# Optimization experiments

Measured on AMD Instinct MI355X. Metric: run time of the kernel, lower is better.

Reference implementation:

```python
import jax, jax.numpy as jnp
import numpy as np

N_NODES = 50000
N_EDGES = 800000
IN_DIM, HID_DIM, OUT_DIM = 64, 128, 128


def _glorot(key, shape):
    fan_in, fan_out = shape[1], shape[0]
    lim = float(np.sqrt(6.0 / (fan_in + fan_out)))
    return jax.random.uniform(key, shape, jnp.float32, -lim, lim)


def setup_inputs() -> dict:
    key = jax.random.key(0)
    ks = jax.random.split(key, 8)
    x = jax.random.normal(ks[0], (N_NODES, IN_DIM), jnp.float32)
    edge_index = jax.random.randint(ks[1], (2, N_EDGES), 0, N_NODES, jnp.int64)
    return {
        "x": x,
        "edge_index": edge_index,
        # layer 1 (SAGEConv: lin_l acts on aggregated neighbors + bias, lin_r on root)
        "W1_l": _glorot(ks[2], (HID_DIM, IN_DIM)),
        "W1_r": _glorot(ks[3], (HID_DIM, IN_DIM)),
        "b1": jnp.zeros((HID_DIM,), jnp.float32),
        # layer 2
        "W2_l": _glorot(ks[4], (OUT_DIM, HID_DIM)),
        "W2_r": _glorot(ks[5], (OUT_DIM, HID_DIM)),
        "b2": jnp.zeros((OUT_DIM,), jnp.float32),
    }


def _sage_conv(x, src, dst, W_l, W_r, b):
    # mean aggregation of neighbor features: messages flow src -> dst
    msg = x[src]                                           # [E, D]
    agg = jax.ops.segment_sum(msg, dst, num_segments=N_NODES)  # [N, D]
    deg = jax.ops.segment_sum(jnp.ones((msg.shape[0],), x.dtype), dst,
                              num_segments=N_NODES)        # [N]
    mean = agg / jnp.maximum(deg, 1.0)[:, None]            # isolated nodes -> 0
    return mean @ W_l.T + x @ W_r.T + b


def reference(x, edge_index, W1_l, W1_r, b1, W2_l, W2_r, b2):
    src, dst = edge_index[0], edge_index[1]
    h = _sage_conv(x, src, dst, W1_l, W1_r, b1)
    h = jax.nn.relu(h)
    out = _sage_conv(h, src, dst, W2_l, W2_r, b2)
    return out
```

## Files before the change

### kernel.cpp

```cpp
#include <hip/hip_runtime.h>
#include <hip/hip_bf16.h>

constexpr int N  = 50000;
constexpr int E  = 800000;
constexpr int D0 = 64;
constexpr int D1 = 128;

constexpr int SB   = 7;
constexpr int SC   = 16;
constexpr int BSTR = 128;

constexpr int NPART = 8;
constexpr int PSZ   = (N + NPART - 1) / NPART;
constexpr int BPP   = 128;

typedef __attribute__((ext_vector_type(8))) short short8;
typedef __attribute__((ext_vector_type(4))) float f32x4;

__device__ __forceinline__ unsigned short bf16bits(float f) {
    __hip_bfloat16 hb = __float2bfloat16(f);
    return *reinterpret_cast<unsigned short*>(&hb);
}

__device__ __forceinline__ void acc8(float* a, const uint4 r) {
    union { unsigned u; float f; } c;
    c.u = r.x << 16;         a[0] += c.f;
    c.u = r.x & 0xffff0000u; a[1] += c.f;
    c.u = r.y << 16;         a[2] += c.f;
    c.u = r.y & 0xffff0000u; a[3] += c.f;
    c.u = r.z << 16;         a[4] += c.f;
    c.u = r.z & 0xffff0000u; a[5] += c.f;
    c.u = r.w << 16;         a[6] += c.f;
    c.u = r.w & 0xffff0000u; a[7] += c.f;
}

__global__ __launch_bounds__(256)
void k_prep(const float* __restrict__ x, unsigned short* __restrict__ xb,
            const float* __restrict__ W1l, const float* __restrict__ W1r,
            const float* __restrict__ W2l, const float* __restrict__ W2r,
            unsigned short* __restrict__ W1cat, unsigned short* __restrict__ W2cat,
            int* __restrict__ cnt8) {
    int i = blockIdx.x * blockDim.x + threadIdx.x;
    if (i < N * 8 / 4) ((int4*)cnt8)[i] = make_int4(0, 0, 0, 0);
    if (i < 128 * 128) {
        int o = i >> 7, k = i & 127;
        float v = (k < 64) ? W1l[o * 64 + k] : W1r[o * 64 + (k - 64)];
        W1cat[i] = bf16bits(v);
    }
    if (i < 128 * 256) {
        int o = i >> 8, k = i & 255;
        float v = (k < 128) ? W2l[o * 128 + k] : W2r[o * 128 + (k - 128)];
        W2cat[i] = bf16bits(v);
    }
    if (i < N * D0 / 8) {
        const float4 v0 = *(const float4*)&x[(size_t)i * 8];
        const float4 v1 = *(const float4*)&x[(size_t)i * 8 + 4];
        float f[8] = {v0.x, v0.y, v0.z, v0.w, v1.x, v1.y, v1.z, v1.w};
        unsigned short u[8];
        #pragma unroll
        for (int j = 0; j < 8; ++j) u[j] = bf16bits(f[j]);
        *(short8*)&xb[(size_t)i * 8] = *(short8*)u;
    }
}

__global__ __launch_bounds__(256)
void k_bin(const int* __restrict__ src, const int* __restrict__ dst,
           int* __restrict__ cnt8, unsigned short* __restrict__ bin) {
    const int p     = blockIdx.x & (NPART - 1);
    const int local = blockIdx.x >> 3;
    const int lo = p * PSZ;
    const int hi = min(N, lo + PSZ);

    for (int i = local * 256 + threadIdx.x; i < E / 4; i += BPP * 256) {
        const int e0 = i * 4;
        int4 d = *(const int4*)&dst[e0];
        int4 s = *(const int4*)&src[e0];
        if (d.x >= lo && d.x < hi) {
            int sb = s.x >> 13;
            int pos = atomicAdd(&cnt8[d.x * 8 + sb], 1);
            if (pos < SC) bin[(size_t)d.x * BSTR + sb * SC + pos] = (unsigned short)s.x;
        }
        if (d.y >= lo && d.y < hi) {
            int sb = s.y >> 13;
            int pos = atomicAdd(&cnt8[d.y * 8 + sb], 1);
            if (pos < SC) bin[(size_t)d.y * BSTR + sb * SC + pos] = (unsigned short)s.y;
        }
        if (d.z >= lo && d.z < hi) {
            int sb = s.z >> 13;
            int pos = atomicAdd(&cnt8[d.z * 8 + sb], 1);
            if (pos < SC) bin[(size_t)d.z * BSTR + sb * SC + pos] = (unsigned short)s.z;
        }
        if (d.w >= lo && d.w < hi) {
            int sb = s.w >> 13;
            int pos = atomicAdd(&cnt8[d.w * 8 + sb], 1);
            if (pos < SC) bin[(size_t)d.w * BSTR + sb * SC + pos] = (unsigned short)s.w;
        }
    }
}

template<int DIN, int NT, bool RELU, bool OUT_BF16>
__global__ __launch_bounds__(256)
void k_layer(const unsigned short* __restrict__ xin,
             const int* __restrict__ cnt8,
             const unsigned short* __restrict__ bin,
             const unsigned short* __restrict__ Wcat,
             const float* __restrict__ bias,
             void* __restrict__ out,
             int n_nodes) {
    constexpr int K  = 2 * DIN;
    constexpr int KP = K + 8;
    __shared__ unsigned short A[NT * KP];

    const int tid   = threadIdx.x;
    const int nbase = blockIdx.x * NT;

    constexpr int CPR = DIN / 8;
    for (int c = tid; c < NT * CPR; c += 256) {
        int row  = c / CPR;
        int col8 = (c - row * CPR) * 8;
        int n    = nbase + row;
        short8 v = (short8)0;
        if (n < n_nodes) v = *(const short8*)&xin[(size_t)n * DIN + col8];
        *(short8*)&A[row * KP + DIN + col8] = v;
    }

    {
        constexpr int GRPSZ = DIN / 8;
        constexpr int NGRP  = 256 / GRPSZ;
        constexpr int NPG   = NT / NGRP;
        const int sub      = tid & (GRPSZ - 1);
        const int gloc     = tid / GRPSZ;
        const int lane     = tid & 63;
        const int lanebase = (lane / GRPSZ) * GRPSZ;

        float a[NPG][8];
        int   dg[NPG];
        #pragma unroll
        for (int i = 0; i < NPG; ++i) {
            dg[i] = 0;
            #pragma unroll
            for (int q = 0; q < 8; ++q) a[i][q] = 0.0f;
        }

        for (int sb = 0; sb < SB; ++sb) {
            #pragma unroll
            for (int i = 0; i < NPG; ++i) {
                const int row = gloc * NPG + i;
                const int n   = nbase + row;
                if (n < n_nodes) {
                    const int raw = cnt8[n * 8 + sb];
                    dg[i] += raw;
                    const int c = min(raw, SC);
                    const size_t base = (size_t)n * BSTR + sb * SC;
                    for (int b = 0; b < c; b += GRPSZ) {
                        int nb = (b + sub < c) ? (int)bin[base + b + sub] : 0;
                        const int cc = min(GRPSZ, c - b);
                        int j = 0;
                        for (; j + 4 <= cc; j += 4) {
                            int s0 = __shfl(nb, lanebase + j + 0);
                            int s1 = __shfl(nb, lanebase + j + 1);
                            int s2 = __shfl(nb, lanebase + j + 2);
                            int s3 = __shfl(nb, lanebase + j + 3);
                            uint4 r0 = *(const uint4*)&xin[(size_t)s0 * DIN + sub * 8];
                            uint4 r1 = *(const uint4*)&xin[(size_t)s1 * DIN + sub * 8];
                            uint4 r2 = *(const uint4*)&xin[(size_t)s2 * DIN + sub * 8];
                            uint4 r3 = *(const uint4*)&xin[(size_t)s3 * DIN + sub * 8];
                            acc8(a[i], r0); acc8(a[i], r1); acc8(a[i], r2); acc8(a[i], r3);
                        }
                        for (; j < cc; ++j) {
                            int s = __shfl(nb, lanebase + j);
                            uint4 r = *(const uint4*)&xin[(size_t)s * DIN + sub * 8];
                            acc8(a[i], r);
                        }
                    }
                }
            }
            __syncthreads();
        }

        #pragma unroll
        for (int i = 0; i < NPG; ++i) {
            const int row = gloc * NPG + i;
            const float invd = 1.0f / fmaxf((float)dg[i], 1.0f);
            unsigned short u[8];
            #pragma unroll
            for (int q = 0; q < 8; ++q) u[q] = bf16bits(a[i][q] * invd);
            *(short8*)&A[row * KP + sub * 8] = *(short8*)u;
        }
    }
    __syncthreads();

    constexpr int WR  = NT / 16;
    constexpr int NCG = 4 / WR;
    constexpr int OT  = 8 / NCG;
    const int lane = tid & 63;
    const int wv   = tid >> 6;
    const int wr   = wv % WR;
    const int wc   = wv / WR;
    const int l15  = lane & 15;
    const int kseg = lane >> 4;

    f32x4 acc[OT];
    #pragma unroll
    for (int ot = 0; ot < OT; ++ot) acc[ot] = (f32x4){0.f, 0.f, 0.f, 0.f};

    #pragma unroll
    for (int kk = 0; kk < K / 32; ++kk) {
        short8 av = *(const short8*)&A[(wr * 16 + l15) * KP + kk * 32 + kseg * 8];
        #pragma unroll
        for (int ot = 0; ot < OT; ++ot) {
            const int o16 = wc * OT + ot;
            short8 b = *(const short8*)&Wcat[(size_t)(o16 * 16 + l15) * K + kk * 32 + kseg * 8];
            acc[ot] = __builtin_amdgcn_mfma_f32_16x16x32_bf16(av, b, acc[ot], 0, 0, 0);
        }
    }

    #pragma unroll
    for (int ot = 0; ot < OT; ++ot) {
        const int o  = (wc * OT + ot) * 16 + l15;
        const float bv = bias[o];
        #pragma unroll
        for (int i = 0; i < 4; ++i) {
            int n = nbase + wr * 16 + kseg * 4 + i;
            if (n < n_nodes) {
                float v = acc[ot][i] + bv;
                if constexpr (RELU) v = fmaxf(v, 0.0f);
                if constexpr (OUT_BF16) {
                    ((unsigned short*)out)[(size_t)n * 128 + o] = bf16bits(v);
                } else {
                    ((float*)out)[(size_t)n * 128 + o] = v;
                }
            }
        }
    }
}

extern "C" void kernel_launch(void* const* d_in, const int* in_sizes, int n_in,
                              void* d_out, int out_size, void* d_ws, size_t ws_size,
                              hipStream_t stream) {
    const float* x   = (const float*)d_in[0];
    const int*   ei  = (const int*)d_in[1];
    const float* W1l = (const float*)d_in[2];
    const float* W1r = (const float*)d_in[3];
    const float* b1  = (const float*)d_in[4];
    const float* W2l = (const float*)d_in[5];
    const float* W2r = (const float*)d_in[6];
    const float* b2  = (const float*)d_in[7];
    float*       out = (float*)d_out;

    const int* src = ei;
    const int* dst = ei + E;

    char* p = (char*)d_ws;
    auto alloc = [&](size_t bytes) -> char* {
        char* r = p; p += (bytes + 15) & ~(size_t)15; return r;
    };
    int*            cnt8  = (int*)alloc((size_t)N * 8 * sizeof(int));
    unsigned short* bin   = (unsigned short*)alloc((size_t)N * BSTR * 2);
    unsigned short* xb    = (unsigned short*)alloc((size_t)N * D0 * 2);
    unsigned short* h     = (unsigned short*)alloc((size_t)N * D1 * 2);
    unsigned short* W1cat = (unsigned short*)alloc(128 * 128 * 2);
    unsigned short* W2cat = (unsigned short*)alloc(128 * 256 * 2);

    k_prep<<<(N * D0 / 8 + 255) / 256, 256, 0, stream>>>(
        x, xb, W1l, W1r, W2l, W2r, W1cat, W2cat, cnt8);

    k_bin<<<NPART * BPP, 256, 0, stream>>>(src, dst, cnt8, bin);

    k_layer<D0, 64, true, true>
        <<<(N + 63) / 64, 256, 0, stream>>>(xb, cnt8, bin, W1cat, b1, h, N);

    k_layer<D1, 32, false, false>
        <<<(N + 31) / 32, 256, 0, stream>>>(h, cnt8, bin, W2cat, b2, out, N);
}
```

Measured before the change: 187.6 us.

## Compact per-node neighbor bins and drop per-subbucket block syncs in aggregation

Adds a k_compact kernel that packs each node's seven source-bucketed neighbor slots into a contiguous list and stores the total degree plus compacted length in one int. The layer kernels then gather over one contiguous list per node, with one count read per node and no __syncthreads between source buckets. This removes the fragmented short loops and the block-wide barriers, which had also kept the gathers loosely in source-bucket order across the block. The cost is an extra launch plus a strided in-place copy pass over the bin array, and some loss of that cache locality.

```diff
diff --git a/kernel.cpp b/kernel.cpp
--- a/kernel.cpp
+++ b/kernel.cpp
@@ -98,10 +98,32 @@
     }
 }
 
+__global__ __launch_bounds__(256)
+void k_compact(const int* __restrict__ cnt8, unsigned short* __restrict__ bin,
+               int* __restrict__ cntc) {
+    int n = blockIdx.x * blockDim.x + threadIdx.x;
+    if (n >= N) return;
+    unsigned short* row = bin + (size_t)n * BSTR;
+    int raw_total = 0;
+    int cur = 0;
+    #pragma unroll
+    for (int sb = 0; sb < SB; ++sb) {
+        int raw = cnt8[n * 8 + sb];
+        raw_total += raw;
+        int c = min(raw, SC);
+        int srcoff = sb * SC;
+        if (cur != srcoff) {
+            for (int j = 0; j < c; ++j) row[cur + j] = row[srcoff + j];
+        }
+        cur += c;
+    }
+    cntc[n] = raw_total | (cur << 16);
+}
+
 template<int DIN, int NT, bool RELU, bool OUT_BF16>
 __global__ __launch_bounds__(256)
 void k_layer(const unsigned short* __restrict__ xin,
-             const int* __restrict__ cnt8,
+             const int* __restrict__ cntc,
              const unsigned short* __restrict__ bin,
              const unsigned short* __restrict__ Wcat,
              const float* __restrict__ bias,
@@ -133,58 +155,45 @@
         const int lane     = tid & 63;
         const int lanebase = (lane / GRPSZ) * GRPSZ;
 
-        float a[NPG][8];
-        int   dg[NPG];
         #pragma unroll
         for (int i = 0; i < NPG; ++i) {
-            dg[i] = 0;
-            #pragma unroll
-            for (int q = 0; q < 8; ++q) a[i][q] = 0.0f;
-        }
-
-        for (int sb = 0; sb < SB; ++sb) {
-            #pragma unroll
-            for (int i = 0; i < NPG; ++i) {
-                const int row = gloc * NPG + i;
-                const int n   = nbase + row;
-                if (n < n_nodes) {
-                    const int raw = cnt8[n * 8 + sb];
-                    dg[i] += raw;
-                    const int c = min(raw, SC);
-                    const size_t base = (size_t)n * BSTR + sb * SC;
-                    for (int b = 0; b < c; b += GRPSZ) {
-                        int nb = (b + sub < c) ? (int)bin[base + b + sub] : 0;
-                        const int cc = min(GRPSZ, c - b);
-                        int j = 0;
-                        for (; j + 4 <= cc; j += 4) {
-                            int s0 = __shfl(nb, lanebase + j + 0);
-                            int s1 = __shfl(nb, lanebase + j + 1);
-                            int s2 = __shfl(nb, lanebase + j + 2);
-                            int s3 = __shfl(nb, lanebase + j + 3);
-                            uint4 r0 = *(const uint4*)&xin[(size_t)s0 * DIN + sub * 8];
-                            uint4 r1 = *(const uint4*)&xin[(size_t)s1 * DIN + sub * 8];
-                            uint4 r2 = *(const uint4*)&xin[(size_t)s2 * DIN + sub * 8];
-                            uint4 r3 = *(const uint4*)&xin[(size_t)s3 * DIN + sub * 8];
-                            acc8(a[i], r0); acc8(a[i], r1); acc8(a[i], r2); acc8(a[i], r3);
-                        }
-                        for (; j < cc; ++j) {
-                            int s = __shfl(nb, lanebase + j);
-                            uint4 r = *(const uint4*)&xin[(size_t)s * DIN + sub * 8];
-                            acc8(a[i], r);
-                        }
+            const int row = gloc * NPG + i;
+            const int n   = nbase + row;
+
+            float a[8] = {0.f, 0.f, 0.f, 0.f, 0.f, 0.f, 0.f, 0.f};
+            int deg = 0;
+            if (n < n_nodes) {
+                const int cc = cntc[n];
+                deg = cc & 0xffff;
+                const int clen = cc >> 16;
+                const size_t base = (size_t)n * BSTR;
+                for (int b = 0; b < clen; b += GRPSZ) {
+                    int nb = (b + sub < clen) ? (int)bin[base + b + sub] : 0;
+                    const int c = min(GRPSZ, clen - b);
+                    int j = 0;
+                    for (; j + 4 <= c; j += 4) {
+                        int s0 = __shfl(nb, lanebase + j + 0);
+                        int s1 = __shfl(nb, lanebase + j + 1);
+                        int s2 = __shfl(nb, lanebase + j + 2);
+                        int s3 = __shfl(nb, lanebase + j + 3);
+                        uint4 r0 = *(const uint4*)&xin[(size_t)s0 * DIN + sub * 8];
+                        uint4 r1 = *(const uint4*)&xin[(size_t)s1 * DIN + sub * 8];
+                        uint4 r2 = *(const uint4*)&xin[(size_t)s2 * DIN + sub * 8];
+                        uint4 r3 = *(const uint4*)&xin[(size_t)s3 * DIN + sub * 8];
+                        acc8(a, r0); acc8(a, r1); acc8(a, r2); acc8(a, r3);
+                    }
+                    for (; j < c; ++j) {
+                        int s = __shfl(nb, lanebase + j);
+                        uint4 r = *(const uint4*)&xin[(size_t)s * DIN + sub * 8];
+                        acc8(a, r);
                     }
                 }
             }
-            __syncthreads();
-        }
-
-        #pragma unroll
-        for (int i = 0; i < NPG; ++i) {
-            const int row = gloc * NPG + i;
-            const float invd = 1.0f / fmaxf((float)dg[i], 1.0f);
+
+            const float invd = 1.0f / fmaxf((float)deg, 1.0f);
             unsigned short u[8];
             #pragma unroll
-            for (int q = 0; q < 8; ++q) u[q] = bf16bits(a[i][q] * invd);
+            for (int q = 0; q < 8; ++q) u[q] = bf16bits(a[q] * invd);
             *(short8*)&A[row * KP + sub * 8] = *(short8*)u;
         }
     }
@@ -256,6 +265,7 @@
         char* r = p; p += (bytes + 15) & ~(size_t)15; return r;
     };
     int*            cnt8  = (int*)alloc((size_t)N * 8 * sizeof(int));
+    int*            cntc  = (int*)alloc((size_t)N * sizeof(int));
     unsigned short* bin   = (unsigned short*)alloc((size_t)N * BSTR * 2);
     unsigned short* xb    = (unsigned short*)alloc((size_t)N * D0 * 2);
     unsigned short* h     = (unsigned short*)alloc((size_t)N * D1 * 2);
@@ -266,10 +276,11 @@
         x, xb, W1l, W1r, W2l, W2r, W1cat, W2cat, cnt8);
 
     k_bin<<<NPART * BPP, 256, 0, stream>>>(src, dst, cnt8, bin);
+    k_compact<<<(N + 255) / 256, 256, 0, stream>>>(cnt8, bin, cntc);
 
     k_layer<D0, 64, true, true>
-        <<<(N + 63) / 64, 256, 0, stream>>>(xb, cnt8, bin, W1cat, b1, h, N);
+        <<<(N + 63) / 64, 256, 0, stream>>>(xb, cntc, bin, W1cat, b1, h, N);
 
     k_layer<D1, 32, false, false>
-        <<<(N + 31) / 32, 256, 0, stream>>>(h, cnt8, bin, W2cat, b2, out, N);
-}
+        <<<(N + 31) / 32, 256, 0, stream>>>(h, cntc, bin, W2cat, b2, out, N);
+}
```

Result: faster. 166.6 us (-11.2%).
